# Performance work log

Hardware: AMD Instinct MI355X
Metric: run time of the kernel (lower is better)

The kernel has to match this reference:

```python
import jax, jax.numpy as jnp
import numpy as np

K = 7  # kernel_size


def _patches(x, k):
    # x: [N, C, H, W] -> [K*K, N, C, H, W]; zero-padded local windows in
    # torch.nn.functional.unfold order (kernel positions row-major).
    N, C, H, W = x.shape
    p = k // 2
    xp = jnp.pad(x, ((0, 0), (0, 0), (p, p), (p, p)))
    return jnp.stack([xp[:, :, i:i + H, j:j + W]
                      for i in range(k) for j in range(k)], axis=0)


def setup_inputs() -> dict:
    key = jax.random.key(0)
    k1, k2 = jax.random.split(key)
    x = jax.random.normal(k1, (4, 128, 80, 80), dtype=jnp.float32)
    feat_in = jax.random.normal(k2, (4, 128, 80, 80), dtype=jnp.float32)
    return {"x": x, "feat_in": feat_in}


def reference(x, feat_in):
    N, C, H, W = feat_in.shape
    k2 = K * K
    # theta_x == phi_x == x in the original module.
    phi_p = _patches(x, K)                            # [K2, N, Cq, H, W]
    # local dot products: weight[k, n, h, w] = sum_c phi_window * theta_center
    w = jnp.einsum('knchw,nchw->knhw', phi_p, x)      # [K2, N, H, W]
    # L1-style normalization over the window (plain sum, as in the source)
    w = w / jnp.sum(w, axis=0, keepdims=True)
    feat_p = _patches(feat_in, K)                     # [K2, N, C, H, W]
    out = jnp.einsum('knhw,knchw->nchw', w, feat_p)   # [N, C, H, W]
    pairwise_weight = w.transpose(1, 2, 3, 0).reshape(N * H * W, 1, k2)
    return out, pairwise_weight
```

## Files before the change

kernel.cpp:

```cpp
#include <hip/hip_runtime.h>


namespace {

constexpr int CN = 4, CC = 128, HT = 80, WD = 80;
constexpr int KK = 7, K2 = 49, PD = 3;
constexpr int TW = 16, TH = 4;
constexpr int HROW = 23;
constexpr int HENT = 10 * HROW;
constexpr int HCHUNK = (HENT * 4 + 63) / 64;
constexpr int HPADF = HCHUNK * 64;
constexpr int PLANE = HT * WD;
constexpr int GSTRIDE = 4 * PLANE;
constexpr int OUT_ELEMS = CN * CC * PLANE;
constexpr int NW = 4, GPW = 8;
constexpr int WR = 53;

__device__ __forceinline__ void make_off(int* off, int bx, int by, int lane) {
#pragma unroll
  for (int q = 0; q < HCHUNK; ++q) {
    int f = q * 64 + lane;
    int e = f >> 2;
    if (e > HENT - 1) e = HENT - 1;
    const int ch = f & 3;
    const int r  = e / HROW;
    const int cl = e - r * HROW;
    int gh = by * TH - PD + r;
    gh = gh < 0 ? 0 : (gh > HT - 1 ? HT - 1 : gh);
    int gw = bx * TW - PD + cl;
    gw = gw < 0 ? 0 : (gw > WD - 1 ? WD - 1 : gw);
    off[q] = ch * PLANE + gh * WD + gw;
  }
}

__device__ __forceinline__ void issue_chunks(const float* gbase, const int* off,
                                             float* lds) {
#if __has_builtin(__builtin_amdgcn_global_load_lds)
#pragma unroll
  for (int q = 0; q < HCHUNK; ++q) {
    __builtin_amdgcn_global_load_lds(
        (const __attribute__((address_space(1))) void*)(gbase + off[q]),
        (__attribute__((address_space(3))) void*)(lds + q * 64), 4, 0, 0);
  }
#else
  const int lane = (int)(threadIdx.x & 63);
#pragma unroll
  for (int q = 0; q < HCHUNK; ++q) lds[q * 64 + lane] = gbase[off[q]];
  asm volatile("s_waitcnt lgkmcnt(0)" ::: "memory");
#endif
}

#define WAIT_VM(n_lit)                                      \
  asm volatile("s_waitcnt vmcnt(" #n_lit ")" ::: "memory"); \
  __builtin_amdgcn_sched_barrier(0)

__global__ __launch_bounds__(256) void lnl2d_v6(const float* __restrict__ x,
                                                const float* __restrict__ feat,
                                                float* __restrict__ dout) {
  __shared__ float halo[NW * 4][HPADF];
  __shared__ float wred[64][WR];
  __shared__ float inv[64];

  const int tid  = (int)threadIdx.x;
  const int wv   = tid >> 6;
  const int lane = tid & 63;
  const int tx = lane & (TW - 1), ty = lane >> 4;
  const int bx = (int)blockIdx.x, by = (int)blockIdx.y, n = (int)blockIdx.z;
  const int h = by * TH + ty, w = bx * TW + tx;

  const float* xw = x + (size_t)n * CC * PLANE + (size_t)wv * 32 * PLANE;
  const float* fw = feat + (size_t)n * CC * PLANE + (size_t)wv * 32 * PLANE;
  float* out = dout;
  float* pw  = dout + OUT_ELEMS;

  int off[HCHUNK];
  make_off(off, bx, by, lane);

#pragma unroll
  for (int i = 0; i < (64 * WR + 255) / 256; ++i) {
    const int idx = i * 256 + tid;
    if (idx < 64 * WR) ((float*)wred)[idx] = 0.f;
  }
  __syncthreads();

  float* hb[4] = {halo[wv * 4 + 0], halo[wv * 4 + 1], halo[wv * 4 + 2],
                  halo[wv * 4 + 3]};

  float acc[K2];
#pragma unroll
  for (int k = 0; k < K2; ++k) acc[k] = 0.f;

  auto corr = [&](const float* b) {
    const float4* h4 = (const float4*)b;
    const float4 c4 = h4[(ty + PD) * HROW + tx + PD];
#pragma unroll
    for (int di = 0; di < KK; ++di)
#pragma unroll
      for (int dj = 0; dj < KK; ++dj) {
        const float4 n4 = h4[(ty + di) * HROW + tx + dj];
        acc[di * KK + dj] += c4.x * n4.x + c4.y * n4.y + c4.z * n4.z + c4.w * n4.w;
      }
  };

  issue_chunks(xw + 0 * GSTRIDE, off, hb[0]);
  issue_chunks(xw + 1 * GSTRIDE, off, hb[1]);
  issue_chunks(xw + 2 * GSTRIDE, off, hb[2]);
#pragma unroll
  for (int g = 0; g < GPW; ++g) {
    if (g < GPW - 3) issue_chunks(xw + (g + 3) * GSTRIDE, off, hb[(g + 3) & 3]);
    if (g < GPW - 3)      { WAIT_VM(45); }
    else if (g == GPW - 3){ WAIT_VM(30); }
    else if (g == GPW - 2){ WAIT_VM(15); }
    else                  { WAIT_VM(0); }
    corr(hb[g & 3]);
  }

#pragma unroll
  for (int di = 0; di < KK; ++di)
#pragma unroll
    for (int dj = 0; dj < KK; ++dj) {
      const int hh = h + di - PD, ww = w + dj - PD;
      if ((unsigned)hh >= (unsigned)HT || (unsigned)ww >= (unsigned)WD)
        acc[di * KK + dj] = 0.f;
    }
#pragma unroll
  for (int k = 0; k < K2; ++k) atomicAdd(&wred[lane][k], acc[k]);

  __syncthreads();

  issue_chunks(fw + 0 * GSTRIDE, off, hb[0]);
  issue_chunks(fw + 1 * GSTRIDE, off, hb[1]);
  issue_chunks(fw + 2 * GSTRIDE, off, hb[2]);

  float wk[K2];
  float ssum = 0.f;
#pragma unroll
  for (int k = 0; k < K2; ++k) { wk[k] = wred[lane][k]; ssum += wk[k]; }
  const float invs = 1.0f / ssum;
#pragma unroll
  for (int k = 0; k < K2; ++k) wk[k] *= invs;
  if (wv == 0) inv[lane] = invs;

  float4 ov[GPW];
#pragma unroll
  for (int g = 0; g < GPW; ++g) ov[g] = make_float4(0.f, 0.f, 0.f, 0.f);

#pragma unroll
  for (int g = 0; g < GPW; ++g) {
    if (g < GPW - 3) issue_chunks(fw + (g + 3) * GSTRIDE, off, hb[(g + 3) & 3]);
    if (g < GPW - 3)      { WAIT_VM(45); }
    else if (g == GPW - 3){ WAIT_VM(30); }
    else if (g == GPW - 2){ WAIT_VM(15); }
    else                  { WAIT_VM(0); }
    const float4* h4 = (const float4*)hb[g & 3];
#pragma unroll
    for (int di = 0; di < KK; ++di)
#pragma unroll
      for (int dj = 0; dj < KK; ++dj) {
        const float4 n4 = h4[(ty + di) * HROW + tx + dj];
        const float f = wk[di * KK + dj];
        ov[g].x += f * n4.x; ov[g].y += f * n4.y; ov[g].z += f * n4.z; ov[g].w += f * n4.w;
      }
  }

  const size_t ob = (size_t)n * CC * PLANE + (size_t)wv * 32 * PLANE +
                    (size_t)(h * WD + w);
#pragma unroll
  for (int g = 0; g < GPW; ++g) {
    out[ob + (size_t)(4 * g + 0) * PLANE] = ov[g].x;
    out[ob + (size_t)(4 * g + 1) * PLANE] = ov[g].y;
    out[ob + (size_t)(4 * g + 2) * PLANE] = ov[g].z;
    out[ob + (size_t)(4 * g + 3) * PLANE] = ov[g].w;
  }

  __syncthreads();

#pragma unroll
  for (int r = 0; r < TH; ++r) {
    float* seg = pw + (size_t)(n * PLANE + (by * TH + r) * WD + bx * TW) * K2;
#pragma unroll
    for (int i = 0; i < (TW * K2) / 256; ++i) {
      const int idx = i * 256 + tid;
      const int col = idx / K2, k = idx - col * K2;
      seg[idx] = wred[r * TW + col][k] * inv[r * TW + col];
    }
    const int rem = TW * K2 - 256 * ((TW * K2) / 256);
    if (tid < rem) {
      const int idx = 256 * ((TW * K2) / 256) + tid;
      const int col = idx / K2, k = idx - col * K2;
      seg[idx] = wred[r * TW + col][k] * inv[r * TW + col];
    }
  }
}

}

extern "C" void kernel_launch(void* const* d_in, const int* in_sizes, int n_in,
                              void* d_out, int out_size, void* d_ws, size_t ws_size,
                              hipStream_t stream) {
  const float* x    = (const float*)d_in[0];
  const float* feat = (const float*)d_in[1];
  float* out        = (float*)d_out;
  dim3 grid(WD / TW, HT / TH, CN);
  lnl2d_v6<<<grid, 256, 0, stream>>>(x, feat, out);
}
```

Before: 137.7 us.

## Split channels across eight waves per block with double-buffered halo staging

Doubles the block to 512 threads so eight waves each handle 16 channels (4 channel groups) instead of four waves handling 32. The per-wave LDS ring drops from four halo buffers to two, using a ping-pong prefetch pipeline with depth one. The aim is more in-flight waves per tile and a shorter serial loop per wave. In exchange, the weight reduction now does more LDS atomics per entry, latency hiding per wave is shallower, and the larger block may lower occupancy.

Result: slower. 179.3 us (+30.2%).

```diff
diff --git a/kernel.cpp b/kernel.cpp
--- a/kernel.cpp
+++ b/kernel.cpp
@@ -13,7 +13,7 @@
 constexpr int PLANE = HT * WD;
 constexpr int GSTRIDE = 4 * PLANE;
 constexpr int OUT_ELEMS = CN * CC * PLANE;
-constexpr int NW = 4, GPW = 8;
+constexpr int NW = 8, GPW = 4;
 constexpr int WR = 53;
 
 __device__ __forceinline__ void make_off(int* off, int bx, int by, int lane) {
@@ -54,10 +54,10 @@
   asm volatile("s_waitcnt vmcnt(" #n_lit ")" ::: "memory"); \
   __builtin_amdgcn_sched_barrier(0)
 
-__global__ __launch_bounds__(256) void lnl2d_v6(const float* __restrict__ x,
+__global__ __launch_bounds__(512) void lnl2d_v8(const float* __restrict__ x,
                                                 const float* __restrict__ feat,
                                                 float* __restrict__ dout) {
-  __shared__ float halo[NW * 4][HPADF];
+  __shared__ float halo[NW * 2][HPADF];
   __shared__ float wred[64][WR];
   __shared__ float inv[64];
 
@@ -68,8 +68,8 @@
   const int bx = (int)blockIdx.x, by = (int)blockIdx.y, n = (int)blockIdx.z;
   const int h = by * TH + ty, w = bx * TW + tx;
 
-  const float* xw = x + (size_t)n * CC * PLANE + (size_t)wv * 32 * PLANE;
-  const float* fw = feat + (size_t)n * CC * PLANE + (size_t)wv * 32 * PLANE;
+  const float* xw = x + (size_t)n * CC * PLANE + (size_t)wv * 16 * PLANE;
+  const float* fw = feat + (size_t)n * CC * PLANE + (size_t)wv * 16 * PLANE;
   float* out = dout;
   float* pw  = dout + OUT_ELEMS;
 
@@ -77,14 +77,14 @@
   make_off(off, bx, by, lane);
 
 #pragma unroll
-  for (int i = 0; i < (64 * WR + 255) / 256; ++i) {
-    const int idx = i * 256 + tid;
+  for (int i = 0; i < (64 * WR + 511) / 512; ++i) {
+    const int idx = i * 512 + tid;
     if (idx < 64 * WR) ((float*)wred)[idx] = 0.f;
   }
   __syncthreads();
 
-  float* hb[4] = {halo[wv * 4 + 0], halo[wv * 4 + 1], halo[wv * 4 + 2],
-                  halo[wv * 4 + 3]};
+  float* hb0 = halo[wv * 2 + 0];
+  float* hb1 = halo[wv * 2 + 1];
 
   float acc[K2];
 #pragma unroll
@@ -102,18 +102,11 @@
       }
   };
 
-  issue_chunks(xw + 0 * GSTRIDE, off, hb[0]);
-  issue_chunks(xw + 1 * GSTRIDE, off, hb[1]);
-  issue_chunks(xw + 2 * GSTRIDE, off, hb[2]);
-#pragma unroll
-  for (int g = 0; g < GPW; ++g) {
-    if (g < GPW - 3) issue_chunks(xw + (g + 3) * GSTRIDE, off, hb[(g + 3) & 3]);
-    if (g < GPW - 3)      { WAIT_VM(45); }
-    else if (g == GPW - 3){ WAIT_VM(30); }
-    else if (g == GPW - 2){ WAIT_VM(15); }
-    else                  { WAIT_VM(0); }
-    corr(hb[g & 3]);
-  }
+  issue_chunks(xw + 0 * GSTRIDE, off, hb0);
+  issue_chunks(xw + 1 * GSTRIDE, off, hb1);  WAIT_VM(15);  corr(hb0);
+  issue_chunks(xw + 2 * GSTRIDE, off, hb0);  WAIT_VM(15);  corr(hb1);
+  issue_chunks(xw + 3 * GSTRIDE, off, hb1);  WAIT_VM(15);  corr(hb0);
+  WAIT_VM(0);                                              corr(hb1);
 
 #pragma unroll
   for (int di = 0; di < KK; ++di)
@@ -128,9 +121,7 @@
 
   __syncthreads();
 
-  issue_chunks(fw + 0 * GSTRIDE, off, hb[0]);
-  issue_chunks(fw + 1 * GSTRIDE, off, hb[1]);
-  issue_chunks(fw + 2 * GSTRIDE, off, hb[2]);
+  issue_chunks(fw + 0 * GSTRIDE, off, hb0);
 
   float wk[K2];
   float ssum = 0.f;
@@ -145,25 +136,24 @@
 #pragma unroll
   for (int g = 0; g < GPW; ++g) ov[g] = make_float4(0.f, 0.f, 0.f, 0.f);
 
-#pragma unroll
-  for (int g = 0; g < GPW; ++g) {
-    if (g < GPW - 3) issue_chunks(fw + (g + 3) * GSTRIDE, off, hb[(g + 3) & 3]);
-    if (g < GPW - 3)      { WAIT_VM(45); }
-    else if (g == GPW - 3){ WAIT_VM(30); }
-    else if (g == GPW - 2){ WAIT_VM(15); }
-    else                  { WAIT_VM(0); }
-    const float4* h4 = (const float4*)hb[g & 3];
+  auto agg = [&](const float* b, float4& o) {
+    const float4* h4 = (const float4*)b;
 #pragma unroll
     for (int di = 0; di < KK; ++di)
 #pragma unroll
       for (int dj = 0; dj < KK; ++dj) {
         const float4 n4 = h4[(ty + di) * HROW + tx + dj];
         const float f = wk[di * KK + dj];
-        ov[g].x += f * n4.x; ov[g].y += f * n4.y; ov[g].z += f * n4.z; ov[g].w += f * n4.w;
+        o.x += f * n4.x; o.y += f * n4.y; o.z += f * n4.z; o.w += f * n4.w;
       }
-  }
+  };
 
-  const size_t ob = (size_t)n * CC * PLANE + (size_t)wv * 32 * PLANE +
+  issue_chunks(fw + 1 * GSTRIDE, off, hb1);  WAIT_VM(15);  agg(hb0, ov[0]);
+  issue_chunks(fw + 2 * GSTRIDE, off, hb0);  WAIT_VM(15);  agg(hb1, ov[1]);
+  issue_chunks(fw + 3 * GSTRIDE, off, hb1);  WAIT_VM(15);  agg(hb0, ov[2]);
+  WAIT_VM(0);                                              agg(hb1, ov[3]);
+
+  const size_t ob = (size_t)n * CC * PLANE + (size_t)wv * 16 * PLANE +
                     (size_t)(h * WD + w);
 #pragma unroll
   for (int g = 0; g < GPW; ++g) {
@@ -178,17 +168,15 @@
 #pragma unroll
   for (int r = 0; r < TH; ++r) {
     float* seg = pw + (size_t)(n * PLANE + (by * TH + r) * WD + bx * TW) * K2;
-#pragma unroll
-    for (int i = 0; i < (TW * K2) / 256; ++i) {
-      const int idx = i * 256 + tid;
+    {
+      const int idx = tid;
       const int col = idx / K2, k = idx - col * K2;
       seg[idx] = wred[r * TW + col][k] * inv[r * TW + col];
     }
-    const int rem = TW * K2 - 256 * ((TW * K2) / 256);
-    if (tid < rem) {
-      const int idx = 256 * ((TW * K2) / 256) + tid;
-      const int col = idx / K2, k = idx - col * K2;
-      seg[idx] = wred[r * TW + col][k] * inv[r * TW + col];
+    const int idx2 = 512 + tid;
+    if (idx2 < TW * K2) {
+      const int col = idx2 / K2, k = idx2 - col * K2;
+      seg[idx2] = wred[r * TW + col][k] * inv[r * TW + col];
     }
   }
 }
@@ -202,5 +190,5 @@
   const float* feat = (const float*)d_in[1];
   float* out        = (float*)d_out;
   dim3 grid(WD / TW, HT / TH, CN);
-  lnl2d_v6<<<grid, 256, 0, stream>>>(x, feat, out);
+  lnl2d_v8<<<grid, 512, 0, stream>>>(x, feat, out);
 }
```
